# Optimization experiments

Hardware: AMD Instinct MI355X
Metric: run time of the kernel (lower is better)

Reference implementation:

```python
import jax, jax.numpy as jnp
import numpy as np

T, BATCH, DMODEL, H = 2048, 16, 512, 512


def setup_inputs() -> dict:
    key = jax.random.key(0)
    ks = jax.random.split(key, 8)
    x = jax.random.normal(ks[0], (T, BATCH, DMODEL), jnp.float32)
    # initial carry: (lambda=1, h=0) so the concat trick leaves state untouched
    h0_re = jnp.zeros((1, BATCH, H), jnp.float32)
    h0_im = jnp.zeros((1, BATCH, H), jnp.float32)
    # LRU parameterization (Orvieto et al. 2023): |lambda| in [0.9, 0.99]
    u1 = jax.random.uniform(ks[1], (H,), jnp.float32)
    nu_log = jnp.log(-0.5 * jnp.log(u1 * (0.99 ** 2 - 0.9 ** 2) + 0.9 ** 2))
    theta_log = jnp.log(jax.random.uniform(ks[2], (H,), jnp.float32) * (np.pi / 10) + 1e-4)
    B_re = jax.random.normal(ks[3], (H, DMODEL), jnp.float32) / np.sqrt(2 * DMODEL)
    B_im = jax.random.normal(ks[4], (H, DMODEL), jnp.float32) / np.sqrt(2 * DMODEL)
    C_re = jax.random.normal(ks[5], (DMODEL, H), jnp.float32) / np.sqrt(H)
    C_im = jax.random.normal(ks[6], (DMODEL, H), jnp.float32) / np.sqrt(H)
    D_vec = jax.random.normal(ks[7], (DMODEL,), jnp.float32)
    return dict(x=x, h0_re=h0_re, h0_im=h0_im, nu_log=nu_log, theta_log=theta_log,
                B_re=B_re, B_im=B_im, C_re=C_re, C_im=C_im, D_vec=D_vec)


def _binop(qi, qj):
    # associative combine for h_t = a_t * h_{t-1} + b_t
    a_i, b_i = qi
    a_j, b_j = qj
    return (a_j * a_i, a_j * b_i + b_j)


def reference(x, h0_re, h0_im, nu_log, theta_log, B_re, B_im, C_re, C_im, D_vec):
    # diagonal complex recurrence eigenvalues, |Lambda| = exp(-exp(nu_log)) < 1
    Lam = jnp.exp(-jnp.exp(nu_log) + 1j * jnp.exp(theta_log))        # [H] complex64
    gamma = jnp.sqrt(1.0 - jnp.exp(-2.0 * jnp.exp(nu_log)))           # [H]
    Bmat = (B_re + 1j * B_im) * gamma[:, None]                         # [H, D]
    # map_to_h: Bu elements and broadcast Lambda elements
    Bu = jnp.einsum('tbd,hd->tbh', x.astype(jnp.complex64), Bmat)      # [T, B, H]
    Lam_el = jnp.broadcast_to(Lam, Bu.shape)                            # [T, B, H]
    # concat previous state (lambda=1, b=h0) as first scan element
    h0 = (h0_re + 1j * h0_im).astype(jnp.complex64)                    # [1, B, H]
    a = jnp.concatenate([jnp.ones_like(h0), Lam_el], axis=0)          # [T+1, B, H]
    b = jnp.concatenate([h0, Bu], axis=0)                              # [T+1, B, H]
    _, h_all = jax.lax.associative_scan(_binop, (a, b), axis=0)
    h = h_all[1:]                                                       # [T, B, H]
    # map_from_h: y = Re(C h) + D * x (elementwise skip)
    Cmat = C_re + 1j * C_im                                             # [D, H]
    y = jnp.einsum('tbh,dh->tbd', h, Cmat).real + D_vec * x            # [T, B, D]
    final_state = h[-1:]                                                # [1, B, H]
    return (final_state, y)
```

## Files before the change

kernel.cpp:

```cpp
#include <hip/hip_runtime.h>
#include <stdint.h>

typedef short shortx8 __attribute__((ext_vector_type(8)));
typedef float floatx4 __attribute__((ext_vector_type(4)));

#define T_LEN 2048
#define BATCH 16
#define DMODEL 512
#define HDIM 512
#define M_ROWS (T_LEN * BATCH)
#define NCHUNK 32
#define LCHUNK 64
#define NCHAIN (BATCH * HDIM)
#define Y_ELEMS (M_ROWS * DMODEL)

__device__ __forceinline__ unsigned short f2bf(float f) {
    union { float f; unsigned u; } v; v.f = f;
    unsigned r = (v.u + 0x7FFFu + ((v.u >> 16) & 1u)) >> 16;
    return (unsigned short)r;
}
__device__ __forceinline__ float bf2f(unsigned short u) {
    union { unsigned u; float f; } v; v.u = ((unsigned)u) << 16;
    return v.f;
}

__global__ void prep_kernel(const float* __restrict__ nu_log, const float* __restrict__ th_log,
                            float* lam_re, float* lam_im, float* l64_re, float* l64_im, float* gam) {
    int h = blockIdx.x * blockDim.x + threadIdx.x;
    if (h >= HDIM) return;
    double nu  = exp((double)nu_log[h]);
    double th  = exp((double)th_log[h]);
    double mag = exp(-nu);
    double lre = mag * cos(th), lim = mag * sin(th);
    double g   = sqrt(1.0 - exp(-2.0 * nu));
    double zr = lre, zi = lim;
    for (int i = 0; i < 6; ++i) { double nr = zr*zr - zi*zi; zi = 2.0*zr*zi; zr = nr; }
    lam_re[h] = (float)lre; lam_im[h] = (float)lim;
    l64_re[h] = (float)zr;  l64_im[h] = (float)zi;
    gam[h] = (float)g;
}

__global__ void conv_BC_kernel(const float* __restrict__ B_re, const float* __restrict__ B_im,
                               const float* __restrict__ gam,
                               const float* __restrict__ C_re, const float* __restrict__ C_im,
                               unsigned short* __restrict__ Bs, unsigned short* __restrict__ C2) {
    int idx = blockIdx.x * blockDim.x + threadIdx.x;
    if (idx < 524288) {
        int n = idx >> 9;
        int d = idx & 511;
        int h = n >> 1;
        float v = ((n & 1) ? B_im[h * DMODEL + d] : B_re[h * DMODEL + d]) * gam[h];
        Bs[idx] = f2bf(v);
    } else {
        int i2 = idx - 524288;
        int d = i2 >> 10;
        int k = i2 & 1023;
        int h = k >> 1;
        float v = (k & 1) ? -C_im[d * HDIM + h] : C_re[d * HDIM + h];
        C2[i2] = f2bf(v);
    }
}

__global__ void cast_x_kernel(const float4* __restrict__ x4, unsigned short* __restrict__ xb, int n4) {
    int i = blockIdx.x * blockDim.x + threadIdx.x;
    if (i >= n4) return;
    float4 v = x4[i];
    ushort4 u;
    u.x = f2bf(v.x); u.y = f2bf(v.y); u.z = f2bf(v.z); u.w = f2bf(v.w);
    *(ushort4*)(xb + (size_t)i * 4) = u;
}

template <int MODE>
__global__ __launch_bounds__(256, 4) void gemm_nt(const unsigned short* __restrict__ A,
                                                  const unsigned short* __restrict__ Bmat,
                                                  const int K, const int N, const int lgNB,
                                                  unsigned short* __restrict__ OutB,
                                                  float* __restrict__ OutF,
                                                  const float* __restrict__ Dv,
                                                  const unsigned short* __restrict__ Xb) {
    __shared__ unsigned short As[128 * 64];
    __shared__ unsigned short Bs[128 * 64];
    const int L = blockIdx.x;
    const int xcd = L & 7;
    const int slot = L >> 3;
    const int bn = slot & ((1 << lgNB) - 1);
    const int bm = xcd * 32 + (slot >> lgNB);
    const int tid = threadIdx.x;
    const int wv = tid >> 6, lane = tid & 63;
    const int wr = wv >> 1, wc = wv & 1;
    const int lrow = lane & 15, qq = lane >> 4;
    floatx4 acc[4][4] = {};

    const size_t rowA = (size_t)bm * 128, rowB = (size_t)bn * 128;
    for (int k0 = 0; k0 < K; k0 += 64) {
        #pragma unroll
        for (int j = 0; j < 4; ++j) {
            int ch  = j * 256 + wv * 64 + lane;
            int r   = ch >> 3;
            int c16 = ch & 7;
            int g16 = c16 ^ (r & 7);
            const unsigned short* ga = A    + (rowA + r) * (size_t)K + (k0 + g16 * 8);
            const unsigned short* gb = Bmat + (rowB + r) * (size_t)K + (k0 + g16 * 8);
            unsigned short* la = As + (size_t)(j * 256 + wv * 64) * 8;
            unsigned short* lb = Bs + (size_t)(j * 256 + wv * 64) * 8;
            __builtin_amdgcn_global_load_lds((const __attribute__((address_space(1))) void*)ga,
                                             (__attribute__((address_space(3))) void*)la, 16, 0, 0);
            __builtin_amdgcn_global_load_lds((const __attribute__((address_space(1))) void*)gb,
                                             (__attribute__((address_space(3))) void*)lb, 16, 0, 0);
        }
        __syncthreads();
        #pragma unroll
        for (int s = 0; s < 2; ++s) {
            shortx8 af[4], bf[4];
            #pragma unroll
            for (int mi = 0; mi < 4; ++mi) {
                int row = wr * 64 + mi * 16 + lrow;
                int c16 = (s * 4 + qq) ^ (row & 7);
                af[mi] = *(const shortx8*)&As[row * 64 + c16 * 8];
            }
            #pragma unroll
            for (int ni = 0; ni < 4; ++ni) {
                int row = wc * 64 + ni * 16 + lrow;
                int c16 = (s * 4 + qq) ^ (row & 7);
                bf[ni] = *(const shortx8*)&Bs[row * 64 + c16 * 8];
            }
            #pragma unroll
            for (int mi = 0; mi < 4; ++mi)
                #pragma unroll
                for (int ni = 0; ni < 4; ++ni)
                    acc[mi][ni] = __builtin_amdgcn_mfma_f32_16x16x32_bf16(af[mi], bf[ni], acc[mi][ni], 0, 0, 0);
        }
        __syncthreads();
    }

    #pragma unroll
    for (int mi = 0; mi < 4; ++mi) {
        int mbase = bm * 128 + wr * 64 + mi * 16 + qq * 4;
        #pragma unroll
        for (int ni = 0; ni < 4; ++ni) {
            int n = bn * 128 + wc * 64 + ni * 16 + lrow;
            if (MODE == 0) {
                #pragma unroll
                for (int r = 0; r < 4; ++r)
                    OutB[(size_t)(mbase + r) * N + n] = f2bf(acc[mi][ni][r]);
            } else {
                float dv = Dv[n];
                #pragma unroll
                for (int r = 0; r < 4; ++r) {
                    size_t idx = (size_t)(mbase + r) * N + n;
                    OutF[idx] = acc[mi][ni][r] + dv * bf2f(Xb[idx]);
                }
            }
        }
    }
}

__global__ void scan_partial(const unsigned short* __restrict__ Bu,
                             const float* __restrict__ lam_re, const float* __restrict__ lam_im,
                             float2* __restrict__ car) {
    int gid = blockIdx.x * blockDim.x + threadIdx.x;
    int chunk = gid >> 13;
    int idx = gid & 8191;
    int b = idx >> 9, h = idx & 511;
    float lr = lam_re[h], li = lam_im[h];
    float vr = 0.f, vi = 0.f;
    const unsigned short* p = Bu + (size_t)chunk * LCHUNK * BATCH * 1024 + (size_t)b * 1024 + 2 * h;
    #pragma unroll 4
    for (int j = 0; j < LCHUNK; ++j) {
        unsigned w = *(const unsigned*)p;
        float br = bf2f((unsigned short)w), bi = bf2f((unsigned short)(w >> 16));
        float nr = lr * vr - li * vi + br;
        float ni = lr * vi + li * vr + bi;
        vr = nr; vi = ni;
        p += BATCH * 1024;
    }
    car[chunk * NCHAIN + idx] = make_float2(vr, vi);
}

__global__ void scan_apply(unsigned short* __restrict__ Bu,
                           const float* __restrict__ lam_re, const float* __restrict__ lam_im,
                           const float* __restrict__ l64_re, const float* __restrict__ l64_im,
                           const float* __restrict__ h0_re, const float* __restrict__ h0_im,
                           const float2* __restrict__ car,
                           float* __restrict__ out_final, int interleave) {
    int gid = blockIdx.x * blockDim.x + threadIdx.x;
    int chunk = gid >> 13;
    int idx = gid & 8191;
    int b = idx >> 9, h = idx & 511;
    float Lr = l64_re[h], Li = l64_im[h];
    float vr = h0_re[idx], vi = h0_im[idx];
    for (int k = 0; k < chunk; ++k) {
        float2 cv = car[k * NCHAIN + idx];
        float nr = Lr * vr - Li * vi + cv.x;
        float ni = Lr * vi + Li * vr + cv.y;
        vr = nr; vi = ni;
    }
    float lr = lam_re[h], li = lam_im[h];
    unsigned short* p = Bu + (size_t)chunk * LCHUNK * BATCH * 1024 + (size_t)b * 1024 + 2 * h;
    #pragma unroll 4
    for (int j = 0; j < LCHUNK; ++j) {
        unsigned w = *(const unsigned*)p;
        float br = bf2f((unsigned short)w), bi = bf2f((unsigned short)(w >> 16));
        float nr = lr * vr - li * vi + br;
        float ni = lr * vi + li * vr + bi;
        vr = nr; vi = ni;
        *(unsigned*)p = (unsigned)f2bf(vr) | ((unsigned)f2bf(vi) << 16);
        p += BATCH * 1024;
    }
    if (chunk == NCHUNK - 1) {
        if (interleave) {
            out_final[2 * idx]     = vr;
            out_final[2 * idx + 1] = vi;
        } else {
            out_final[idx] = vr;
        }
    }
}

extern "C" void kernel_launch(void* const* d_in, const int* in_sizes, int n_in,
                              void* d_out, int out_size, void* d_ws, size_t ws_size,
                              hipStream_t stream) {
    const float* x        = (const float*)d_in[0];
    const float* h0_re    = (const float*)d_in[1];
    const float* h0_im    = (const float*)d_in[2];
    const float* nu_log   = (const float*)d_in[3];
    const float* theta_lg = (const float*)d_in[4];
    const float* B_re     = (const float*)d_in[5];
    const float* B_im     = (const float*)d_in[6];
    const float* C_re     = (const float*)d_in[7];
    const float* C_im     = (const float*)d_in[8];
    const float* D_vec    = (const float*)d_in[9];

    char* ws = (char*)d_ws;
    unsigned short* BuH  = (unsigned short*)(ws + 0);
    unsigned short* xb   = (unsigned short*)(ws + 67108864);
    unsigned short* Bs   = (unsigned short*)(ws + 100663296);
    unsigned short* C2   = (unsigned short*)(ws + 101711872);
    float2* car          = (float2*)(ws + 102760448);
    float* lam_re        = (float*)(ws + 104857600);
    float* lam_im        = (float*)(ws + 104859648);
    float* l64_re        = (float*)(ws + 104861696);
    float* l64_im        = (float*)(ws + 104863744);
    float* gam           = (float*)(ws + 104865792);

    int fs_elems = out_size - Y_ELEMS;
    int interleave = (fs_elems == 8192) ? 0 : 1;
    if (fs_elems != 8192) fs_elems = 16384;
    float* out_final = (float*)d_out;
    float* y_out     = (float*)d_out + fs_elems;

    prep_kernel<<<2, 256, 0, stream>>>(nu_log, theta_lg, lam_re, lam_im, l64_re, l64_im, gam);
    conv_BC_kernel<<<(1048576) / 256, 256, 0, stream>>>(B_re, B_im, gam, C_re, C_im, Bs, C2);
    cast_x_kernel<<<(Y_ELEMS / 4) / 256, 256, 0, stream>>>((const float4*)x, xb, Y_ELEMS / 4);
    gemm_nt<0><<<2048, 256, 0, stream>>>(xb, Bs, DMODEL, 1024, 3, BuH, nullptr, nullptr, nullptr);
    scan_partial<<<(NCHUNK * NCHAIN) / 256, 256, 0, stream>>>(BuH, lam_re, lam_im, car);
    scan_apply<<<(NCHUNK * NCHAIN) / 256, 256, 0, stream>>>(BuH, lam_re, lam_im, l64_re, l64_im,
                                                            h0_re, h0_im, car,
                                                            out_final, interleave);
    gemm_nt<1><<<1024, 256, 0, stream>>>(BuH, C2, 1024, 512, 2, nullptr, y_out, D_vec, xb);
}
```

Before: 263.5 us.

## Fuse x bf16 cast into GEMM load and merge prep kernels

```diff
diff --git a/kernel.cpp b/kernel.cpp
--- a/kernel.cpp
+++ b/kernel.cpp
@@ -24,60 +24,53 @@
     return v.f;
 }
 
-__global__ void prep_kernel(const float* __restrict__ nu_log, const float* __restrict__ th_log,
-                            float* lam_re, float* lam_im, float* l64_re, float* l64_im, float* gam) {
-    int h = blockIdx.x * blockDim.x + threadIdx.x;
-    if (h >= HDIM) return;
-    double nu  = exp((double)nu_log[h]);
-    double th  = exp((double)th_log[h]);
-    double mag = exp(-nu);
-    double lre = mag * cos(th), lim = mag * sin(th);
-    double g   = sqrt(1.0 - exp(-2.0 * nu));
-    double zr = lre, zi = lim;
-    for (int i = 0; i < 6; ++i) { double nr = zr*zr - zi*zi; zi = 2.0*zr*zi; zr = nr; }
-    lam_re[h] = (float)lre; lam_im[h] = (float)lim;
-    l64_re[h] = (float)zr;  l64_im[h] = (float)zi;
-    gam[h] = (float)g;
-}
-
-__global__ void conv_BC_kernel(const float* __restrict__ B_re, const float* __restrict__ B_im,
-                               const float* __restrict__ gam,
-                               const float* __restrict__ C_re, const float* __restrict__ C_im,
-                               unsigned short* __restrict__ Bs, unsigned short* __restrict__ C2) {
-    int idx = blockIdx.x * blockDim.x + threadIdx.x;
-    if (idx < 524288) {
-        int n = idx >> 9;
-        int d = idx & 511;
-        int h = n >> 1;
-        float v = ((n & 1) ? B_im[h * DMODEL + d] : B_re[h * DMODEL + d]) * gam[h];
-        Bs[idx] = f2bf(v);
+__global__ void conv_all(const float* __restrict__ B_re, const float* __restrict__ B_im,
+                         const float* __restrict__ nu_log, const float* __restrict__ th_log,
+                         const float* __restrict__ C_re, const float* __restrict__ C_im,
+                         unsigned short* __restrict__ Bs, unsigned short* __restrict__ C2,
+                         float* lam_re, float* lam_im, float* l64_re, float* l64_im) {
+    int bid = blockIdx.x;
+    int tid = threadIdx.x;
+    if (bid < 4096) {
+        int idx = bid * 256 + tid;
+        if (idx < 524288) {
+            int n = idx >> 9;
+            int d = idx & 511;
+            int h = n >> 1;
+            float g = sqrtf(1.0f - expf(-2.0f * expf(nu_log[h])));
+            float v = ((n & 1) ? B_im[h * DMODEL + d] : B_re[h * DMODEL + d]) * g;
+            Bs[idx] = f2bf(v);
+        } else {
+            int i2 = idx - 524288;
+            int d = i2 >> 10;
+            int k = i2 & 1023;
+            int h = k >> 1;
+            float v = (k & 1) ? -C_im[d * HDIM + h] : C_re[d * HDIM + h];
+            C2[i2] = f2bf(v);
+        }
     } else {
-        int i2 = idx - 524288;
-        int d = i2 >> 10;
-        int k = i2 & 1023;
-        int h = k >> 1;
-        float v = (k & 1) ? -C_im[d * HDIM + h] : C_re[d * HDIM + h];
-        C2[i2] = f2bf(v);
-    }
-}
-
-__global__ void cast_x_kernel(const float4* __restrict__ x4, unsigned short* __restrict__ xb, int n4) {
-    int i = blockIdx.x * blockDim.x + threadIdx.x;
-    if (i >= n4) return;
-    float4 v = x4[i];
-    ushort4 u;
-    u.x = f2bf(v.x); u.y = f2bf(v.y); u.z = f2bf(v.z); u.w = f2bf(v.w);
-    *(ushort4*)(xb + (size_t)i * 4) = u;
+        for (int h = tid; h < HDIM; h += 256) {
+            double nu  = exp((double)nu_log[h]);
+            double th  = exp((double)th_log[h]);
+            double mag = exp(-nu);
+            double lre = mag * cos(th), lim = mag * sin(th);
+            double zr = lre, zi = lim;
+            for (int i = 0; i < 6; ++i) { double nr = zr*zr - zi*zi; zi = 2.0*zr*zi; zr = nr; }
+            lam_re[h] = (float)lre; lam_im[h] = (float)lim;
+            l64_re[h] = (float)zr;  l64_im[h] = (float)zi;
+        }
+    }
 }
 
 template <int MODE>
 __global__ __launch_bounds__(256, 4) void gemm_nt(const unsigned short* __restrict__ A,
+                                                  const float* __restrict__ Af,
                                                   const unsigned short* __restrict__ Bmat,
                                                   const int K, const int N, const int lgNB,
                                                   unsigned short* __restrict__ OutB,
                                                   float* __restrict__ OutF,
                                                   const float* __restrict__ Dv,
-                                                  const unsigned short* __restrict__ Xb) {
+                                                  const float* __restrict__ Xf) {
     __shared__ unsigned short As[128 * 64];
     __shared__ unsigned short Bs[128 * 64];
     const int L = blockIdx.x;
@@ -93,20 +86,53 @@
 
     const size_t rowA = (size_t)bm * 128, rowB = (size_t)bn * 128;
     for (int k0 = 0; k0 < K; k0 += 64) {
-        #pragma unroll
-        for (int j = 0; j < 4; ++j) {
-            int ch  = j * 256 + wv * 64 + lane;
-            int r   = ch >> 3;
-            int c16 = ch & 7;
-            int g16 = c16 ^ (r & 7);
-            const unsigned short* ga = A    + (rowA + r) * (size_t)K + (k0 + g16 * 8);
-            const unsigned short* gb = Bmat + (rowB + r) * (size_t)K + (k0 + g16 * 8);
-            unsigned short* la = As + (size_t)(j * 256 + wv * 64) * 8;
-            unsigned short* lb = Bs + (size_t)(j * 256 + wv * 64) * 8;
-            __builtin_amdgcn_global_load_lds((const __attribute__((address_space(1))) void*)ga,
-                                             (__attribute__((address_space(3))) void*)la, 16, 0, 0);
-            __builtin_amdgcn_global_load_lds((const __attribute__((address_space(1))) void*)gb,
-                                             (__attribute__((address_space(3))) void*)lb, 16, 0, 0);
+        if (MODE == 0) {
+            float4 va[4][2];
+            #pragma unroll
+            for (int j = 0; j < 4; ++j) {
+                int ch  = j * 256 + tid;
+                int r   = ch >> 3;
+                int g16 = (ch & 7) ^ (r & 7);
+                const float* ga = Af + (rowA + r) * (size_t)K + (k0 + g16 * 8);
+                va[j][0] = *(const float4*)ga;
+                va[j][1] = *(const float4*)(ga + 4);
+            }
+            #pragma unroll
+            for (int j = 0; j < 4; ++j) {
+                int ch  = j * 256 + wv * 64 + lane;
+                int r   = ch >> 3;
+                int g16 = (ch & 7) ^ (r & 7);
+                const unsigned short* gb = Bmat + (rowB + r) * (size_t)K + (k0 + g16 * 8);
+                unsigned short* lb = Bs + (size_t)(j * 256 + wv * 64) * 8;
+                __builtin_amdgcn_global_load_lds((const __attribute__((address_space(1))) void*)gb,
+                                                 (__attribute__((address_space(3))) void*)lb, 16, 0, 0);
+            }
+            #pragma unroll
+            for (int j = 0; j < 4; ++j) {
+                int ch = j * 256 + tid;
+                shortx8 t;
+                t[0] = (short)f2bf(va[j][0].x); t[1] = (short)f2bf(va[j][0].y);
+                t[2] = (short)f2bf(va[j][0].z); t[3] = (short)f2bf(va[j][0].w);
+                t[4] = (short)f2bf(va[j][1].x); t[5] = (short)f2bf(va[j][1].y);
+                t[6] = (short)f2bf(va[j][1].z); t[7] = (short)f2bf(va[j][1].w);
+                *(shortx8*)&As[(size_t)ch * 8] = t;
+            }
+        } else {
+            #pragma unroll
+            for (int j = 0; j < 4; ++j) {
+                int ch  = j * 256 + wv * 64 + lane;
+                int r   = ch >> 3;
+                int c16 = ch & 7;
+                int g16 = c16 ^ (r & 7);
+                const unsigned short* ga = A    + (rowA + r) * (size_t)K + (k0 + g16 * 8);
+                const unsigned short* gb = Bmat + (rowB + r) * (size_t)K + (k0 + g16 * 8);
+                unsigned short* la = As + (size_t)(j * 256 + wv * 64) * 8;
+                unsigned short* lb = Bs + (size_t)(j * 256 + wv * 64) * 8;
+                __builtin_amdgcn_global_load_lds((const __attribute__((address_space(1))) void*)ga,
+                                                 (__attribute__((address_space(3))) void*)la, 16, 0, 0);
+                __builtin_amdgcn_global_load_lds((const __attribute__((address_space(1))) void*)gb,
+                                                 (__attribute__((address_space(3))) void*)lb, 16, 0, 0);
+            }
         }
         __syncthreads();
         #pragma unroll
@@ -148,7 +174,7 @@
                 #pragma unroll
                 for (int r = 0; r < 4; ++r) {
                     size_t idx = (size_t)(mbase + r) * N + n;
-                    OutF[idx] = acc[mi][ni][r] + dv * bf2f(Xb[idx]);
+                    OutF[idx] = acc[mi][ni][r] + dv * Xf[idx];
                 }
             }
         }
@@ -233,7 +259,6 @@
 
     char* ws = (char*)d_ws;
     unsigned short* BuH  = (unsigned short*)(ws + 0);
-    unsigned short* xb   = (unsigned short*)(ws + 67108864);
     unsigned short* Bs   = (unsigned short*)(ws + 100663296);
     unsigned short* C2   = (unsigned short*)(ws + 101711872);
     float2* car          = (float2*)(ws + 102760448);
@@ -241,7 +266,6 @@
     float* lam_im        = (float*)(ws + 104859648);
     float* l64_re        = (float*)(ws + 104861696);
     float* l64_im        = (float*)(ws + 104863744);
-    float* gam           = (float*)(ws + 104865792);
 
     int fs_elems = out_size - Y_ELEMS;
     int interleave = (fs_elems == 8192) ? 0 : 1;
@@ -249,13 +273,12 @@
     float* out_final = (float*)d_out;
     float* y_out     = (float*)d_out + fs_elems;
 
-    prep_kernel<<<2, 256, 0, stream>>>(nu_log, theta_lg, lam_re, lam_im, l64_re, l64_im, gam);
-    conv_BC_kernel<<<(1048576) / 256, 256, 0, stream>>>(B_re, B_im, gam, C_re, C_im, Bs, C2);
-    cast_x_kernel<<<(Y_ELEMS / 4) / 256, 256, 0, stream>>>((const float4*)x, xb, Y_ELEMS / 4);
-    gemm_nt<0><<<2048, 256, 0, stream>>>(xb, Bs, DMODEL, 1024, 3, BuH, nullptr, nullptr, nullptr);
+    conv_all<<<4097, 256, 0, stream>>>(B_re, B_im, nu_log, theta_lg, C_re, C_im,
+                                       Bs, C2, lam_re, lam_im, l64_re, l64_im);
+    gemm_nt<0><<<2048, 256, 0, stream>>>(nullptr, x, Bs, DMODEL, 1024, 3, BuH, nullptr, nullptr, nullptr);
     scan_partial<<<(NCHUNK * NCHAIN) / 256, 256, 0, stream>>>(BuH, lam_re, lam_im, car);
     scan_apply<<<(NCHUNK * NCHAIN) / 256, 256, 0, stream>>>(BuH, lam_re, lam_im, l64_re, l64_im,
                                                             h0_re, h0_im, car,
                                                             out_final, interleave);
-    gemm_nt<1><<<1024, 256, 0, stream>>>(BuH, C2, 1024, 512, 2, nullptr, y_out, D_vec, xb);
-}
+    gemm_nt<1><<<1024, 256, 0, stream>>>(BuH, nullptr, C2, 1024, 512, 2, nullptr, y_out, D_vec, x);
+}
```

Result: slower. 281.6 us (+6.9%).
